# Kernel optimization log

Hardware: AMD Instinct MI355X
Metric: run time of the kernel (lower is better)

Reference implementation:

```python
import jax, jax.numpy as jnp
import numpy as np


def setup_inputs() -> dict:
    key = jax.random.key(0)
    ks = jax.random.split(key, 5)
    B, C, W, H = 8, 256, 64, 64
    d = C // 8  # query/key channels per SAGAN k=8
    s = 1.0 / np.sqrt(C)
    return {
        "x": jax.random.normal(ks[0], (B, C, W, H), dtype=jnp.float32),
        "wq": jax.random.normal(ks[1], (d, C), dtype=jnp.float32) * s,
        "bq": jnp.zeros((d,), dtype=jnp.float32),
        "wk": jax.random.normal(ks[2], (d, C), dtype=jnp.float32) * s,
        "bk": jnp.zeros((d,), dtype=jnp.float32),
        "wv": jax.random.normal(ks[3], (C, C), dtype=jnp.float32) * s,
        "bv": jnp.zeros((C,), dtype=jnp.float32),
        # gamma is init to 0 in torch; set to 1 so the attention branch is active
        "gamma": jnp.ones((1,), dtype=jnp.float32),
    }


def reference(x, wq, bq, wk, bk, wv, bv, gamma):
    B, C, W, H = x.shape
    N = W * H
    xf = x.reshape(B, C, N)  # spatial tokens flattened
    # 1x1 convs == per-token channel matmuls
    q = jnp.einsum('dc,bcn->bdn', wq, xf) + bq[None, :, None]  # [B, d, N]
    k = jnp.einsum('dc,bcn->bdn', wk, xf) + bk[None, :, None]  # [B, d, N]
    v = jnp.einsum('ec,bcn->ben', wv, xf) + bv[None, :, None]  # [B, C, N]
    # attention_map[b,i,j] = softmax_j( sum_d k[b,d,i] * q[b,d,j] )
    scores = jnp.einsum('bdi,bdj->bij', k, q)  # [B, N, N]
    attention_map = jax.nn.softmax(scores, axis=-1)
    # attention_out[b,c,n] = sum_m v[b,c,m] * A[b,m,n]
    attention_out = jnp.einsum('bcm,bmn->bcn', v, attention_map).reshape(B, C, W, H)
    out = gamma * attention_out + x
    return out, attention_map
```

## Files before the change

### kernel.cpp

```cpp
#include <hip/hip_runtime.h>

#define B 8
#define C 256
#define NN 4096

typedef float f32x4 __attribute__((ext_vector_type(4)));
typedef short s16x8 __attribute__((ext_vector_type(8)));
typedef unsigned short u16;
typedef unsigned int u32;

__device__ __forceinline__ u16 f2bf(float f) {
    u32 u = __builtin_bit_cast(u32, f);
    u32 r = (u + 0x7fffu + ((u >> 16) & 1u)) >> 16;
    return (u16)r;
}
__device__ __forceinline__ float bf2f(u16 h) {
    u32 u = ((u32)h) << 16;
    return __builtin_bit_cast(float, u);
}

__device__ __forceinline__ void bar_lds() {
    asm volatile("s_waitcnt lgkmcnt(0)\n\ts_barrier" ::: "memory");
}

#define MFMA(a, b, c) __builtin_amdgcn_mfma_f32_16x16x32_bf16((a), (b), (c), 0, 0, 0)

__device__ __forceinline__ f32x4 score_mfma_t(s16x8 aqh, s16x8 aql, s16x8 bkh, s16x8 bkl) {
    f32x4 s = {0.f, 0.f, 0.f, 0.f};
    s = MFMA(aqh, bkl, s);
    s = MFMA(aql, bkh, s);
    s = MFMA(aqh, bkh, s);
    return s;
}

__global__ void k_sentinel(float* __restrict__ out, float v) { out[0] = v; }

__global__ void k_cast(const float* __restrict__ wv, const float* __restrict__ wq,
                       const float* __restrict__ wk, u16* __restrict__ wvb,
                       u16* __restrict__ wqh, u16* __restrict__ wql,
                       u16* __restrict__ wkh, u16* __restrict__ wkl) {
    int i = blockIdx.x * 256 + threadIdx.x;
    if (i < 65536) {
        int e = i & 7, lan = (i >> 3) & 15, g = (i >> 7) & 3, ck = (i >> 9) & 7, es = i >> 12;
        wvb[i] = f2bf(wv[(es * 16 + lan) * 256 + ck * 32 + g * 8 + e]);
    } else if (i < 73728) {
        int j = i - 65536;
        int e = j & 7, lan = (j >> 3) & 15, g = (j >> 7) & 3, ck = (j >> 9) & 7, es = j >> 12;
        float v = wq[(es * 16 + lan) * 256 + ck * 32 + g * 8 + e];
        u16 h = f2bf(v); wqh[j] = h; wql[j] = f2bf(v - bf2f(h));
    } else {
        int j = i - 73728;
        int e = j & 7, lan = (j >> 3) & 15, g = (j >> 7) & 3, ck = (j >> 9) & 7, es = j >> 12;
        float v = wk[(es * 16 + lan) * 256 + ck * 32 + g * 8 + e];
        u16 h = f2bf(v); wkh[j] = h; wkl[j] = f2bf(v - bf2f(h));
    }
}

__global__ __launch_bounds__(256) void k_proj(
    const float* __restrict__ x,
    const u16* __restrict__ wvb, const float* __restrict__ bv,
    const u16* __restrict__ wqh, const u16* __restrict__ wql, const float* __restrict__ bq,
    const u16* __restrict__ wkh, const u16* __restrict__ wkl, const float* __restrict__ bk,
    u16* __restrict__ vbf,
    u16* __restrict__ qh, u16* __restrict__ ql, u16* __restrict__ kh, u16* __restrict__ kl)
{
    __shared__ u16 smh[64 * 264];
    __shared__ u16 sml[64 * 264];
    int t = threadIdx.x;
    int w = t >> 6, l = t & 63;
    int lan = l & 15, g = l >> 4;
    int b = blockIdx.x, nblk = blockIdx.y;
    int n0 = nblk * 64;
#pragma unroll
    for (int p = 0; p < 16; p++) {
        int flat4 = t + p * 256;
        int c = flat4 >> 4, n4 = (flat4 & 15) * 4;
        float4 xv = *(const float4*)&x[((size_t)b * C + c) * NN + n0 + n4];
        float vv[4] = {xv.x, xv.y, xv.z, xv.w};
#pragma unroll
        for (int j = 0; j < 4; j++) {
            u16 h = f2bf(vv[j]);
            smh[(n4 + j) * 264 + c] = h;
            sml[(n4 + j) * 264 + c] = f2bf(vv[j] - bf2f(h));
        }
    }
    __syncthreads();
    f32x4 accv[16];
    f32x4 accq[2], acck[2];
#pragma unroll
    for (int es = 0; es < 16; es++) accv[es] = {0.f, 0.f, 0.f, 0.f};
#pragma unroll
    for (int es = 0; es < 2; es++) { accq[es] = {0.f, 0.f, 0.f, 0.f}; acck[es] = {0.f, 0.f, 0.f, 0.f}; }
    int nrow = w * 16 + lan;
    for (int ck = 0; ck < 8; ck++) {
        int c0 = ck * 32 + g * 8;
        int fb = ((ck * 4 + g) * 16 + lan) * 8;
        s16x8 bh = *(const s16x8*)&smh[nrow * 264 + c0];
        s16x8 bl = *(const s16x8*)&sml[nrow * 264 + c0];
#pragma unroll
        for (int es = 0; es < 16; es++) {
            s16x8 afrag = *(const s16x8*)&wvb[es * 4096 + fb];
            accv[es] = MFMA(afrag, bh, accv[es]);
        }
#pragma unroll
        for (int es = 0; es < 2; es++) {
            s16x8 ah = *(const s16x8*)&wqh[es * 4096 + fb];
            s16x8 al = *(const s16x8*)&wql[es * 4096 + fb];
            accq[es] = MFMA(ah, bl, accq[es]);
            accq[es] = MFMA(al, bh, accq[es]);
            accq[es] = MFMA(ah, bh, accq[es]);
            ah = *(const s16x8*)&wkh[es * 4096 + fb];
            al = *(const s16x8*)&wkl[es * 4096 + fb];
            acck[es] = MFMA(ah, bl, acck[es]);
            acck[es] = MFMA(al, bh, acck[es]);
            acck[es] = MFMA(ah, bh, acck[es]);
        }
    }
    int ncol = n0 + w * 16 + lan;
#pragma unroll
    for (int es = 0; es < 16; es++)
#pragma unroll
        for (int r = 0; r < 4; r++) {
            int e = es * 16 + g * 4 + r;
            vbf[((size_t)b * C + e) * NN + ncol] = f2bf(accv[es][r] + bv[e]);
        }
    bar_lds();
    u16* sqk = sml;
    int nloc = w * 16 + lan;
#pragma unroll
    for (int es = 0; es < 2; es++)
#pragma unroll
        for (int r = 0; r < 4; r++) {
            int d = es * 16 + g * 4 + r;
            float qv = accq[es][r] + bq[d];
            float kv = acck[es][r] + bk[d];
            u16 qhi = f2bf(qv); u16 qlo = f2bf(qv - bf2f(qhi));
            u16 khi = f2bf(kv); u16 klo = f2bf(kv - bf2f(khi));
            sqk[nloc * 136 + 0 * 32 + d] = qhi;
            sqk[nloc * 136 + 1 * 32 + d] = qlo;
            sqk[nloc * 136 + 2 * 32 + d] = khi;
            sqk[nloc * 136 + 3 * 32 + d] = klo;
        }
    bar_lds();
    {
        int n = t >> 2, arr = t & 3;
        const u16* src = &sqk[n * 136 + arr * 32];
        u16* dst = (arr == 0 ? qh : arr == 1 ? ql : arr == 2 ? kh : kl) + ((size_t)b * NN + n0 + n) * 32;
        uint4 v0 = *(const uint4*)&src[0];
        uint4 v1 = *(const uint4*)&src[8];
        uint4 v2 = *(const uint4*)&src[16];
        uint4 v3 = *(const uint4*)&src[24];
        *(uint4*)&dst[0]  = v0;
        *(uint4*)&dst[8]  = v1;
        *(uint4*)&dst[16] = v2;
        *(uint4*)&dst[24] = v3;
    }
}

__global__ __launch_bounds__(256) void k_zsum(
    const u16* __restrict__ qh, const u16* __restrict__ ql,
    const u16* __restrict__ kh, const u16* __restrict__ kl,
    float* __restrict__ zinv)
{
    __shared__ float lZ[4][64];
    int t = threadIdx.x;
    int w = t >> 6, l = t & 63;
    int lan = l & 15, g = l >> 4;
    int b = blockIdx.x, mblk = blockIdx.y;
    int m0 = mblk * 64;

    s16x8 bkh[4], bkl[4];
#pragma unroll
    for (int ms = 0; ms < 4; ms++) {
        size_t ko = ((size_t)b * NN + m0 + ms * 16 + lan) * 32 + g * 8;
        bkh[ms] = *(const s16x8*)&kh[ko];
        bkl[ms] = *(const s16x8*)&kl[ko];
    }
    float zacc[4] = {0.f, 0.f, 0.f, 0.f};
    for (int ci = 0; ci < 64; ci++) {
        int nt = ci * 4 + w;
        size_t qo = ((size_t)b * NN + nt * 16 + lan) * 32 + g * 8;
        s16x8 aqh = *(const s16x8*)&qh[qo];
        s16x8 aql = *(const s16x8*)&ql[qo];
#pragma unroll
        for (int ms = 0; ms < 4; ms++) {
            f32x4 s = score_mfma_t(aqh, aql, bkh[ms], bkl[ms]);
            zacc[ms] += __expf(s[0]) + __expf(s[1]) + __expf(s[2]) + __expf(s[3]);
        }
    }
#pragma unroll
    for (int ms = 0; ms < 4; ms++) {
        float v = zacc[ms];
        v += __shfl_xor(v, 16);
        v += __shfl_xor(v, 32);
        zacc[ms] = v;
    }
    if (g == 0) {
#pragma unroll
        for (int ms = 0; ms < 4; ms++) lZ[w][ms * 16 + lan] = zacc[ms];
    }
    __syncthreads();
    if (t < 64) {
        float Z = lZ[0][t] + lZ[1][t] + lZ[2][t] + lZ[3][t];
        zinv[(size_t)b * NN + m0 + t] = 1.0f / Z;
    }
}

__global__ __launch_bounds__(256) void k_attn2(
    const float* __restrict__ x,
    const u16* __restrict__ qh, const u16* __restrict__ ql,
    const u16* __restrict__ kh, const u16* __restrict__ kl,
    const u16* __restrict__ vbf, const float* __restrict__ zinv,
    const float* __restrict__ gamma,
    float* __restrict__ out, float* __restrict__ amap)
{
    __shared__ u16 smv[16384];
    __shared__ u16 mn[64 * 68];
    int t = threadIdx.x;
    int w = t >> 6, l = t & 63;
    int lan = l & 15, g = l >> 4;
    int b = blockIdx.x, nblk = blockIdx.y;
    int n0 = nblk * 64;
    int nw = n0 + w * 16;

    size_t qo = ((size_t)b * NN + nw + lan) * 32 + g * 8;
    s16x8 aqh = *(const s16x8*)&qh[qo];
    s16x8 aql = *(const s16x8*)&ql[qo];

    f32x4 acc[16];
#pragma unroll
    for (int cs = 0; cs < 16; cs++) acc[cs] = {0.f, 0.f, 0.f, 0.f};
    const u16* vb = vbf + (size_t)b * C * NN;
    const float* ziv = zinv + (size_t)b * NN;
    float* amp = amap + (size_t)b * NN * NN;

    s16x8 vreg[8];
#pragma unroll
    for (int p = 0; p < 8; p++) {
        int f8 = t + p * 256; int c = f8 >> 3, j = f8 & 7;
        vreg[p] = *(const s16x8*)&vb[(size_t)c * NN + j * 8];
    }
#pragma unroll
    for (int p = 0; p < 8; p++) {
        int f8 = t + p * 256; int c = f8 >> 3, j = f8 & 7;
        *(s16x8*)&smv[c * 64 + ((j ^ (c & 7)) * 8)] = vreg[p];
    }
    bar_lds();

    for (int mstep = 0; mstep < 64; mstep++) {
        int m0 = mstep * 64;
#pragma unroll
        for (int ms = 0; ms < 4; ms++) {
            size_t ko = ((size_t)b * NN + m0 + ms * 16 + lan) * 32 + g * 8;
            s16x8 fkh = *(const s16x8*)&kh[ko];
            s16x8 fkl = *(const s16x8*)&kl[ko];
            f32x4 s = score_mfma_t(aqh, aql, fkh, fkl);
            float zi = ziv[m0 + ms * 16 + lan];
            uint2 pk;
            pk.x = (u32)f2bf(__expf(s[0]) * zi) | ((u32)f2bf(__expf(s[1]) * zi) << 16);
            pk.y = (u32)f2bf(__expf(s[2]) * zi) | ((u32)f2bf(__expf(s[3]) * zi) << 16);
            *(uint2*)&mn[(ms * 16 + lan) * 68 + w * 16 + g * 4] = pk;
        }
        bar_lds();
        if (mstep < 63) {
#pragma unroll
            for (int p = 0; p < 8; p++) {
                int f8 = t + p * 256; int c = f8 >> 3, j = f8 & 7;
                vreg[p] = *(const s16x8*)&vb[(size_t)c * NN + m0 + 64 + j * 8];
            }
        }
#pragma unroll
        for (int p = 0; p < 4; p++) {
            int mm = p * 16 + (t >> 4);
            int c4 = (t & 15) * 4;
            uint2 pk = *(const uint2*)&mn[mm * 68 + c4];
            f32x4 v;
            v[0] = bf2f((u16)(pk.x & 0xffff)); v[1] = bf2f((u16)(pk.x >> 16));
            v[2] = bf2f((u16)(pk.y & 0xffff)); v[3] = bf2f((u16)(pk.y >> 16));
            __builtin_nontemporal_store(v, (f32x4*)&amp[(size_t)(m0 + mm) * NN + n0 + c4]);
        }
#pragma unroll
        for (int ks = 0; ks < 2; ks++) {
            s16x8 bfrag;
#pragma unroll
            for (int e = 0; e < 8; e++)
                bfrag[e] = (short)mn[(ks * 32 + g * 8 + e) * 68 + w * 16 + lan];
#pragma unroll
            for (int cs = 0; cs < 16; cs++) {
                int row = cs * 16 + lan;
                s16x8 afrag = *(const s16x8*)&smv[row * 64 + (((ks * 4 + g) ^ (lan & 7)) * 8)];
                acc[cs] = MFMA(afrag, bfrag, acc[cs]);
            }
        }
        bar_lds();
        if (mstep < 63) {
#pragma unroll
            for (int p = 0; p < 8; p++) {
                int f8 = t + p * 256; int c = f8 >> 3, j = f8 & 7;
                *(s16x8*)&smv[c * 64 + ((j ^ (c & 7)) * 8)] = vreg[p];
            }
        }
    }
    float gm = gamma[0];
    int ncol = nw + lan;
#pragma unroll
    for (int cs = 0; cs < 16; cs++)
#pragma unroll
        for (int r = 0; r < 4; r++) {
            int c = cs * 16 + g * 4 + r;
            size_t oi = ((size_t)b * C + c) * NN + ncol;
            out[oi] = gm * acc[cs][r] + x[oi];
        }
}

extern "C" void kernel_launch(void* const* d_in, const int* in_sizes, int n_in,
                              void* d_out, int out_size, void* d_ws, size_t ws_size,
                              hipStream_t stream) {
    const float* x     = (const float*)d_in[0];
    const float* wq    = (const float*)d_in[1];
    const float* bq    = (const float*)d_in[2];
    const float* wk    = (const float*)d_in[3];
    const float* bk    = (const float*)d_in[4];
    const float* wv    = (const float*)d_in[5];
    const float* bv    = (const float*)d_in[6];
    const float* gamma = (const float*)d_in[7];
    float* out  = (float*)d_out;
    float* amap = out + (size_t)B * C * NN;

    const size_t WS_NEED = (size_t)26 << 20;
    if (ws_size < WS_NEED) {
        k_sentinel<<<dim3(1), dim3(1), 0, stream>>>(out, 8.0e7f);
        return;
    }
    if (n_in < 8 || in_sizes[0] != B * C * NN || in_sizes[1] != 32 * C ||
        in_sizes[2] != 32 || in_sizes[3] != 32 * C || in_sizes[4] != 32 ||
        in_sizes[5] != C * C || in_sizes[6] != C || in_sizes[7] != 1) {
        k_sentinel<<<dim3(1), dim3(1), 0, stream>>>(out, 9.0e7f);
        return;
    }

    unsigned char* ws = (unsigned char*)d_ws;
    u16* qh   = (u16*)(ws);
    u16* ql   = (u16*)(ws + ((size_t)2 << 20));
    u16* kh   = (u16*)(ws + ((size_t)4 << 20));
    u16* kl   = (u16*)(ws + ((size_t)6 << 20));
    u16* vbf  = (u16*)(ws + ((size_t)8 << 20));
    float* zinv = (float*)(ws + ((size_t)24 << 20));
    u16* wvb  = (u16*)(ws + ((size_t)25 << 20));
    u16* wqh  = (u16*)(ws + ((size_t)25 << 20) + (128 << 10));
    u16* wql  = (u16*)(ws + ((size_t)25 << 20) + (144 << 10));
    u16* wkh  = (u16*)(ws + ((size_t)25 << 20) + (160 << 10));
    u16* wkl  = (u16*)(ws + ((size_t)25 << 20) + (176 << 10));

    k_cast<<<dim3(320), dim3(256), 0, stream>>>(wv, wq, wk, wvb, wqh, wql, wkh, wkl);
    k_proj<<<dim3(8, 64), dim3(256), 0, stream>>>(x, wvb, bv, wqh, wql, bq, wkh, wkl, bk,
                                                  vbf, qh, ql, kh, kl);
    k_zsum<<<dim3(8, 64), dim3(256), 0, stream>>>(qh, ql, kh, kl, zinv);
    k_attn2<<<dim3(8, 64), dim3(256), 0, stream>>>(x, qh, ql, kh, kl, vbf, zinv, gamma, out, amap);
}
```

Before: 268.9 us.

## Re-tile PV matmul so each wave owns 64 channels across all 64 columns

The P·V accumulation changes from each wave covering all 256 channels for its own 16 columns to each wave covering 64 channels across all 64 columns of the block, as a 4x4 MFMA tile. A transposed copy of the probability tile is written to a new LDS buffer so B fragments load as vectors instead of eight scalar gathers. Each V fragment read from LDS is now reused across four MFMAs, which cuts LDS read traffic. In exchange there is extra LDS usage and four scalar LDS stores per score tile to fill the transposed buffer.

```diff
diff --git a/kernel.cpp b/kernel.cpp
--- a/kernel.cpp
+++ b/kernel.cpp
@@ -216,6 +216,7 @@
 {
     __shared__ u16 smv[16384];
     __shared__ u16 mn[64 * 68];
+    __shared__ u16 nm[64 * 80];
     int t = threadIdx.x;
     int w = t >> 6, l = t & 63;
     int lan = l & 15, g = l >> 4;
@@ -227,9 +228,12 @@
     s16x8 aqh = *(const s16x8*)&qh[qo];
     s16x8 aql = *(const s16x8*)&ql[qo];
 
-    f32x4 acc[16];
-#pragma unroll
-    for (int cs = 0; cs < 16; cs++) acc[cs] = {0.f, 0.f, 0.f, 0.f};
+    f32x4 acc[4][4];
+#pragma unroll
+    for (int ct = 0; ct < 4; ct++)
+#pragma unroll
+        for (int nt = 0; nt < 4; nt++) acc[ct][nt] = {0.f, 0.f, 0.f, 0.f};
+
     const u16* vb = vbf + (size_t)b * C * NN;
     const float* ziv = zinv + (size_t)b * NN;
     float* amp = amap + (size_t)b * NN * NN;
@@ -256,10 +260,19 @@
             s16x8 fkl = *(const s16x8*)&kl[ko];
             f32x4 s = score_mfma_t(aqh, aql, fkh, fkl);
             float zi = ziv[m0 + ms * 16 + lan];
+            u16 b0 = f2bf(__expf(s[0]) * zi);
+            u16 b1 = f2bf(__expf(s[1]) * zi);
+            u16 b2 = f2bf(__expf(s[2]) * zi);
+            u16 b3 = f2bf(__expf(s[3]) * zi);
             uint2 pk;
-            pk.x = (u32)f2bf(__expf(s[0]) * zi) | ((u32)f2bf(__expf(s[1]) * zi) << 16);
-            pk.y = (u32)f2bf(__expf(s[2]) * zi) | ((u32)f2bf(__expf(s[3]) * zi) << 16);
+            pk.x = (u32)b0 | ((u32)b1 << 16);
+            pk.y = (u32)b2 | ((u32)b3 << 16);
             *(uint2*)&mn[(ms * 16 + lan) * 68 + w * 16 + g * 4] = pk;
+            int nr = w * 16 + g * 4;
+            nm[(nr + 0) * 80 + ms * 16 + lan] = b0;
+            nm[(nr + 1) * 80 + ms * 16 + lan] = b1;
+            nm[(nr + 2) * 80 + ms * 16 + lan] = b2;
+            nm[(nr + 3) * 80 + ms * 16 + lan] = b3;
         }
         bar_lds();
         if (mstep < 63) {
@@ -281,15 +294,17 @@
         }
 #pragma unroll
         for (int ks = 0; ks < 2; ks++) {
-            s16x8 bfrag;
-#pragma unroll
-            for (int e = 0; e < 8; e++)
-                bfrag[e] = (short)mn[(ks * 32 + g * 8 + e) * 68 + w * 16 + lan];
-#pragma unroll
-            for (int cs = 0; cs < 16; cs++) {
-                int row = cs * 16 + lan;
-                s16x8 afrag = *(const s16x8*)&smv[row * 64 + (((ks * 4 + g) ^ (lan & 7)) * 8)];
-                acc[cs] = MFMA(afrag, bfrag, acc[cs]);
+            s16x8 bfr[4];
+#pragma unroll
+            for (int nt = 0; nt < 4; nt++)
+                bfr[nt] = *(const s16x8*)&nm[(nt * 16 + lan) * 80 + ks * 32 + g * 8];
+#pragma unroll
+            for (int ct = 0; ct < 4; ct++) {
+                int row = w * 64 + ct * 16 + lan;
+                s16x8 af = *(const s16x8*)&smv[row * 64 + (((ks * 4 + g) ^ (lan & 7)) * 8)];
+#pragma unroll
+                for (int nt = 0; nt < 4; nt++)
+                    acc[ct][nt] = MFMA(af, bfr[nt], acc[ct][nt]);
             }
         }
         bar_lds();
@@ -302,15 +317,16 @@
         }
     }
     float gm = gamma[0];
-    int ncol = nw + lan;
-#pragma unroll
-    for (int cs = 0; cs < 16; cs++)
-#pragma unroll
-        for (int r = 0; r < 4; r++) {
-            int c = cs * 16 + g * 4 + r;
-            size_t oi = ((size_t)b * C + c) * NN + ncol;
-            out[oi] = gm * acc[cs][r] + x[oi];
-        }
+#pragma unroll
+    for (int ct = 0; ct < 4; ct++)
+#pragma unroll
+        for (int nt = 0; nt < 4; nt++)
+#pragma unroll
+            for (int r = 0; r < 4; r++) {
+                int c = w * 64 + ct * 16 + g * 4 + r;
+                size_t oi = ((size_t)b * C + c) * NN + n0 + nt * 16 + lan;
+                out[oi] = gm * acc[ct][nt][r] + x[oi];
+            }
 }
 
 extern "C" void kernel_launch(void* const* d_in, const int* in_sizes, int n_in,
```

Result: slower. 290.2 us (+7.9%).
